# Kernel tuning notes

Hardware: AMD Instinct MI355X
Metric: run time of the kernel (lower is better)

## Reference

```python
import jax, jax.numpy as jnp
import numpy as np

N, T, D, H, W = 2, 1024, 1024, 16, 64  # batch, seq, embed, heads, temporal_window
DH = D // H                             # head_dim = 64
WIN = 2 * W + 1                         # 129


def setup_inputs() -> dict:
    key = jax.random.key(0)
    ks = jax.random.split(key, 10)
    s = 0.02
    inp = {"x": jax.random.normal(ks[0], (N, T, D), jnp.float32)}
    inp["w_q"] = jax.random.normal(ks[1], (D, D), jnp.float32) * s
    inp["b_q"] = jnp.zeros((D,), jnp.float32)
    inp["w_k"] = jax.random.normal(ks[2], (D, D), jnp.float32) * s
    inp["b_k"] = jnp.zeros((D,), jnp.float32)
    inp["w_v"] = jax.random.normal(ks[3], (D, D), jnp.float32) * s
    inp["b_v"] = jnp.zeros((D,), jnp.float32)
    inp["w_o"] = jax.random.normal(ks[4], (D, D), jnp.float32) * s
    inp["b_o"] = jnp.zeros((D,), jnp.float32)
    return inp


def reference(x, w_q, b_q, w_k, b_k, w_v, b_v, w_o, b_o):
    # x: (N, T, D). Windowed MHA: query t attends to positions [t-W, t+W].
    n, t_len, d = x.shape
    scale = 1.0 / jnp.sqrt(jnp.asarray(DH, x.dtype))

    q = (x @ w_q.T + b_q).reshape(n, t_len, H, DH)
    k = (x @ w_k.T + b_k).reshape(n, t_len, H, DH)
    v = (x @ w_v.T + b_v).reshape(n, t_len, H, DH)

    # window index map: pos[t, r] = t + r - W  (r in [0, 2W])
    t_idx = jnp.arange(t_len)[:, None]
    r_idx = jnp.arange(WIN)[None, :]
    pos = t_idx + r_idx - W
    valid = (pos >= 0) & (pos < t_len)
    idx = jnp.clip(pos, 0, t_len - 1)

    k_win = k[:, idx]
    v_win = v[:, idx]

    scores = jnp.einsum('nthd,ntwhd->nhtw', q, k_win) * scale
    scores = jnp.where(valid[None, None], scores, -jnp.inf)
    p = jax.nn.softmax(scores, axis=-1)

    out = jnp.einsum('nhtw,ntwhd->nthd', p, v_win).reshape(n, t_len, d)
    return out @ w_o.T + b_o
```

## Files before the change

### kernel.cpp

```cpp
#include <hip/hip_runtime.h>
#include <hip/hip_fp16.h>
#include <cstdint>
#include <cstddef>

using f16x8  = _Float16 __attribute__((ext_vector_type(8)));
using f16x4  = _Float16 __attribute__((ext_vector_type(4)));
using f32x4  = float __attribute__((ext_vector_type(4)));
using f32x16 = float __attribute__((ext_vector_type(16)));

#define GLDS16(g, l) __builtin_amdgcn_global_load_lds(                        \
    (const __attribute__((address_space(1))) void*)(g),                       \
    (__attribute__((address_space(3))) void*)(l), 16, 0, 0)

__device__ inline void cast4(const float* __restrict__ in,
                             _Float16* __restrict__ out, int i) {
  float4 v = reinterpret_cast<const float4*>(in)[i];
  f16x4 h;
  h[0] = (_Float16)v.x; h[1] = (_Float16)v.y;
  h[2] = (_Float16)v.z; h[3] = (_Float16)v.w;
  reinterpret_cast<f16x4*>(out)[i] = h;
}

__global__ void prep_kernel(const float* __restrict__ x,
                            const float* __restrict__ wq, const float* __restrict__ wk,
                            const float* __restrict__ wv, const float* __restrict__ wo,
                            const float* __restrict__ bq, const float* __restrict__ bk,
                            const float* __restrict__ bv,
                            _Float16* __restrict__ xh, _Float16* __restrict__ wcat,
                            _Float16* __restrict__ woh, float* __restrict__ bcat) {
  int i = blockIdx.x * blockDim.x + threadIdx.x;
  const int XU = 512 * 1024;
  const int WU = 256 * 1024;
  if (i < XU) { cast4(x, xh, i); return; }
  i -= XU;
  if (i < WU) { cast4(wq, wcat, i); return; }
  i -= WU;
  if (i < WU) { cast4(wk, wcat + 1024 * 1024, i); return; }
  i -= WU;
  if (i < WU) { cast4(wv, wcat + 2 * 1024 * 1024, i); return; }
  i -= WU;
  if (i < WU) { cast4(wo, woh, i); return; }
  i -= WU;
  if (i < 256) { reinterpret_cast<float4*>(bcat)[i] = reinterpret_cast<const float4*>(bq)[i]; return; }
  i -= 256;
  if (i < 256) { reinterpret_cast<float4*>(bcat + 1024)[i] = reinterpret_cast<const float4*>(bk)[i]; return; }
  i -= 256;
  if (i < 256) { reinterpret_cast<float4*>(bcat + 2048)[i] = reinterpret_cast<const float4*>(bv)[i]; return; }
}

template <int BM, int BN, typename TOUT>
__global__ __launch_bounds__(256, 4) void gemm_bt(
    const _Float16* __restrict__ A, const _Float16* __restrict__ B,
    const float* __restrict__ bias, TOUT* __restrict__ C,
    int M, int N, int K) {
  constexpr int AR = BM / 32;
  constexpr int BR = BN / 32;
  constexpr int MI = BM / 64;
  constexpr int NI = BN / 64;
  __shared__ _Float16 As[BM * 64];
  __shared__ _Float16 Bs[BN * 64];

  const int tid  = threadIdx.x;
  const int lane = tid & 63;
  const int wave = tid >> 6;
  const int l31  = lane & 31;
  const int half = lane >> 5;
  const int lsw  = l31 & 7;

  const int nlin = blockIdx.y * gridDim.x + blockIdx.x;
  const int xcd  = nlin & 7;
  const int slot = nlin >> 3;
  const int cpx  = gridDim.x >> 3;
  const int bx   = xcd * cpx + (slot % cpx);
  const int by   = slot / cpx;

  const int m0 = by * BM;
  const int n0 = bx * BN;
  const int wr = (wave >> 1) * (BM / 2);
  const int wc = (wave & 1) * (BN / 2);

  const int srow = tid >> 3;
  const int skun = (tid & 7) ^ (srow & 7);
  const _Float16* Ag[AR];
  const _Float16* Bg[BR];
#pragma unroll
  for (int r = 0; r < AR; r++) Ag[r] = A + (size_t)(m0 + 32 * r + srow) * K + skun * 8;
#pragma unroll
  for (int r = 0; r < BR; r++) Bg[r] = B + (size_t)(n0 + 32 * r + srow) * K + skun * 8;

  f32x16 acc[MI][NI];
#pragma unroll
  for (int i = 0; i < MI; i++)
#pragma unroll
    for (int j = 0; j < NI; j++) acc[i][j] = (f32x16)0.0f;

  for (int kt = 0; kt < K; kt += 64) {
    __syncthreads();
#pragma unroll
    for (int r = 0; r < AR; r++) GLDS16(Ag[r] + kt, &As[(256 * r + tid) * 8]);
#pragma unroll
    for (int r = 0; r < BR; r++) GLDS16(Bg[r] + kt, &Bs[(256 * r + tid) * 8]);
    __syncthreads();

#pragma unroll
    for (int ks = 0; ks < 4; ks++) {
      const int ku = ks * 2 + half;
      f16x8 af[MI], bf[NI];
#pragma unroll
      for (int mi = 0; mi < MI; mi++) {
        const int row = wr + mi * 32 + l31;
        af[mi] = *reinterpret_cast<const f16x8*>(&As[(row * 8 + (ku ^ lsw)) * 8]);
      }
#pragma unroll
      for (int ni = 0; ni < NI; ni++) {
        const int col = wc + ni * 32 + l31;
        bf[ni] = *reinterpret_cast<const f16x8*>(&Bs[(col * 8 + (ku ^ lsw)) * 8]);
      }
#pragma unroll
      for (int mi = 0; mi < MI; mi++)
#pragma unroll
        for (int ni = 0; ni < NI; ni++)
          acc[mi][ni] = __builtin_amdgcn_mfma_f32_32x32x16_f16(af[mi], bf[ni], acc[mi][ni], 0, 0, 0);
    }
  }

#pragma unroll
  for (int mi = 0; mi < MI; mi++) {
    const int rbase = m0 + wr + mi * 32 + 4 * half;
#pragma unroll
    for (int ni = 0; ni < NI; ni++) {
      const int col = n0 + wc + ni * 32 + l31;
      const float bv = bias ? bias[col] : 0.f;
#pragma unroll
      for (int r = 0; r < 16; r++) {
        const int row = rbase + (r & 3) + 8 * (r >> 2);
        C[(size_t)row * N + col] = (TOUT)(acc[mi][ni][r] + bv);
      }
    }
  }
}

#define T_LEN 1024
#define KSTR 72
#define VSTR 200

__global__ __launch_bounds__(256) void attn_win(
    const _Float16* __restrict__ qkv, _Float16* __restrict__ o) {
  __shared__ _Float16 KP[192 * KSTR];
  __shared__ _Float16 Vt[64 * VSTR];

  const int b  = blockIdx.x;
  const int qt = b & 15;
  const int h  = (b >> 4) & 15;
  const int n  = b >> 8;
  const int t0 = qt * 64;

  const int tid  = threadIdx.x;
  const int lane = tid & 63;
  const int wave = tid >> 6;
  const int l15  = lane & 15;
  const int quad = lane >> 4;
  const int jtb  = wave & 2;
  const int ksb  = wave >> 1;

  const size_t rowstr = 3072;
  const _Float16* qbase = qkv + (size_t)n * T_LEN * rowstr + h * 64;
  const _Float16* kbase = qbase + 1024;
  const _Float16* vbase = qbase + 2048;

  const _Float16* qrow = qbase + (size_t)(t0 + wave * 16 + l15) * rowstr;
  const f16x8 qf0 = *reinterpret_cast<const f16x8*>(qrow + quad * 8);
  const f16x8 qf1 = *reinterpret_cast<const f16x8*>(qrow + 32 + quad * 8);

  for (int idx = tid; idx < 192 * 8; idx += 256) {
    const int j  = idx >> 3;
    const int d8 = (idx & 7) * 8;
    const int t  = t0 - 64 + j;
    f16x8 kv;
    if (t >= 0 && t < T_LEN) {
      kv = *reinterpret_cast<const f16x8*>(kbase + (size_t)t * rowstr + d8);
    } else {
      for (int i = 0; i < 8; i++) kv[i] = (_Float16)0.f;
    }
    *reinterpret_cast<f16x8*>(&KP[j * KSTR + d8]) = kv;
  }
  for (int it = 0; it < 6; it++) {
    const int item = it * 256 + tid;
    const int j    = (item & 63) + ((item >> 9) << 6);
    const int dgrp = (item >> 6) & 7;
    const int t = t0 - 64 + j;
    f16x8 vv;
    if (t >= 0 && t < T_LEN) {
      vv = *reinterpret_cast<const f16x8*>(vbase + (size_t)t * rowstr + dgrp * 8);
    } else {
      for (int i = 0; i < 8; i++) vv[i] = (_Float16)0.f;
    }
#pragma unroll
    for (int i = 0; i < 8; i++) Vt[(dgrp * 8 + i) * VSTR + j] = vv[i];
  }
  __syncthreads();

  f32x4 accs[10];
#pragma unroll
  for (int t = 0; t < 10; t++) accs[t] = f32x4{0.f, 0.f, 0.f, 0.f};
#pragma unroll
  for (int t = 0; t < 10; t++) {
    const int jt = jtb + t;
    const f16x8 b0 = *reinterpret_cast<const f16x8*>(&KP[(jt * 16 + l15) * KSTR + quad * 8]);
    const f16x8 b1 = *reinterpret_cast<const f16x8*>(&KP[(jt * 16 + l15) * KSTR + 32 + quad * 8]);
    accs[t] = __builtin_amdgcn_mfma_f32_16x16x32_f16(qf0, b0, accs[t], 0, 0, 0);
    accs[t] = __builtin_amdgcn_mfma_f32_16x16x32_f16(qf1, b1, accs[t], 0, 0, 0);
  }
  __syncthreads();

  float rmax[4] = {-1e30f, -1e30f, -1e30f, -1e30f};
#pragma unroll
  for (int t = 0; t < 10; t++) {
    const int jcol = (jtb + t) * 16 + l15;
    const int tabs = t0 - 64 + jcol;
#pragma unroll
    for (int r = 0; r < 4; r++) {
      const int q = wave * 16 + quad * 4 + r;
      const bool valid = (jcol >= q) && (jcol <= q + 128) && (tabs >= 0) && (tabs < T_LEN);
      const float s = valid ? accs[t][r] * 0.125f : -1e30f;
      accs[t][r] = s;
      rmax[r] = fmaxf(rmax[r], s);
    }
  }
#pragma unroll
  for (int r = 0; r < 4; r++)
#pragma unroll
    for (int m = 1; m < 16; m <<= 1) rmax[r] = fmaxf(rmax[r], __shfl_xor(rmax[r], m));

  float rsum[4] = {0.f, 0.f, 0.f, 0.f};
#pragma unroll
  for (int t = 0; t < 10; t++)
#pragma unroll
    for (int r = 0; r < 4; r++) {
      const float p = __expf(accs[t][r] - rmax[r]);
      accs[t][r] = p;
      rsum[r] += p;
    }
#pragma unroll
  for (int r = 0; r < 4; r++)
#pragma unroll
    for (int m = 1; m < 16; m <<= 1) rsum[r] += __shfl_xor(rsum[r], m);

  _Float16* Pw = &KP[wave * 16 * VSTR];
#pragma unroll
  for (int t = 0; t < 10; t++)
#pragma unroll
    for (int r = 0; r < 4; r++)
      Pw[(quad * 4 + r) * VSTR + (jtb + t) * 16 + l15] = (_Float16)accs[t][r];
  __syncthreads();

  f32x4 acco[4];
#pragma unroll
  for (int ni = 0; ni < 4; ni++) acco[ni] = f32x4{0.f, 0.f, 0.f, 0.f};
#pragma unroll
  for (int ks2 = 0; ks2 < 5; ks2++) {
    const int ks = ksb + ks2;
    const f16x8 pa = *reinterpret_cast<const f16x8*>(&Pw[l15 * VSTR + ks * 32 + quad * 8]);
#pragma unroll
    for (int ni = 0; ni < 4; ni++) {
      const f16x8 vb = *reinterpret_cast<const f16x8*>(&Vt[(ni * 16 + l15) * VSTR + ks * 32 + quad * 8]);
      acco[ni] = __builtin_amdgcn_mfma_f32_16x16x32_f16(pa, vb, acco[ni], 0, 0, 0);
    }
  }

  float rinv[4];
#pragma unroll
  for (int r = 0; r < 4; r++) rinv[r] = 1.f / rsum[r];

  _Float16* obase = o + (size_t)(n * T_LEN + t0 + wave * 16) * 1024 + h * 64;
#pragma unroll
  for (int ni = 0; ni < 4; ni++)
#pragma unroll
    for (int r = 0; r < 4; r++)
      obase[(size_t)(quad * 4 + r) * 1024 + ni * 16 + l15] = (_Float16)(acco[ni][r] * rinv[r]);
}

extern "C" void kernel_launch(void* const* d_in, const int* in_sizes, int n_in,
                              void* d_out, int out_size, void* d_ws, size_t ws_size,
                              hipStream_t stream) {
  const float* x   = (const float*)d_in[0];
  const float* w_q = (const float*)d_in[1];
  const float* b_q = (const float*)d_in[2];
  const float* w_k = (const float*)d_in[3];
  const float* b_k = (const float*)d_in[4];
  const float* w_v = (const float*)d_in[5];
  const float* b_v = (const float*)d_in[6];
  const float* w_o = (const float*)d_in[7];
  const float* b_o = (const float*)d_in[8];
  float* out = (float*)d_out;

  char* ws = (char*)d_ws;
  _Float16* xh   = (_Float16*)(ws);
  _Float16* wcat = (_Float16*)(ws + (4ull << 20));
  _Float16* woh  = (_Float16*)(ws + (10ull << 20));
  _Float16* qkvh = (_Float16*)(ws + (12ull << 20));
  _Float16* oh   = xh;
  float*    bcat = (float*)(ws + (24ull << 20));

  const int PREP_UNITS = 512 * 1024 + 4 * 256 * 1024 + 3 * 256;
  prep_kernel<<<(PREP_UNITS + 255) / 256, 256, 0, stream>>>(
      x, w_q, w_k, w_v, w_o, b_q, b_k, b_v, xh, wcat, woh, bcat);

  gemm_bt<64, 128, _Float16><<<dim3(24, 32), 256, 0, stream>>>(
      xh, wcat, bcat, qkvh, 2048, 3072, 1024);

  attn_win<<<512, 256, 0, stream>>>(qkvh, oh);

  gemm_bt<64, 64, float><<<dim3(16, 32), 256, 0, stream>>>(
      oh, woh, b_o, out, 2048, 1024, 1024);
}
```

Before: 128.7 us.

## Use 2-wave GEMM blocks with wider per-wave tiles and paired V transpose stores

Reworks the GEMM kernel so each block runs 2 waves (128 threads). Each wave now covers the full BM rows and a WN-wide column slice, which gives more MFMA work per wave and more register reuse of fragments. Launch bounds change to match, and the global-to-LDS load loops are re-derived for the smaller thread count. Separately, the attention V transpose now loads two consecutive rows per thread and writes f16x2 pairs into the transposed LDS buffer, halving the number of LDS store instructions. The cost is fewer threads per block issuing loads and larger accumulator register use, which may hurt latency hiding.

```diff
diff --git a/kernel.cpp b/kernel.cpp
--- a/kernel.cpp
+++ b/kernel.cpp
@@ -5,6 +5,7 @@
 
 using f16x8  = _Float16 __attribute__((ext_vector_type(8)));
 using f16x4  = _Float16 __attribute__((ext_vector_type(4)));
+using f16x2  = _Float16 __attribute__((ext_vector_type(2)));
 using f32x4  = float __attribute__((ext_vector_type(4)));
 using f32x16 = float __attribute__((ext_vector_type(16)));
 
@@ -48,15 +49,18 @@
   if (i < 256) { reinterpret_cast<float4*>(bcat + 2048)[i] = reinterpret_cast<const float4*>(bv)[i]; return; }
 }
 
-template <int BM, int BN, typename TOUT>
-__global__ __launch_bounds__(256, 4) void gemm_bt(
+template <int BM, int BN, int WN, typename TOUT>
+__global__ __launch_bounds__((BN / WN) * 64, 2) void gemm_bt(
     const _Float16* __restrict__ A, const _Float16* __restrict__ B,
     const float* __restrict__ bias, TOUT* __restrict__ C,
     int M, int N, int K) {
-  constexpr int AR = BM / 32;
-  constexpr int BR = BN / 32;
-  constexpr int MI = BM / 64;
-  constexpr int NI = BN / 64;
+  constexpr int NW  = BN / WN;
+  constexpr int NT  = NW * 64;
+  constexpr int RPR = NT / 8;
+  constexpr int AR  = BM / RPR;
+  constexpr int BR  = BN / RPR;
+  constexpr int MI  = BM / 32;
+  constexpr int NI  = WN / 32;
   __shared__ _Float16 As[BM * 64];
   __shared__ _Float16 Bs[BN * 64];
 
@@ -76,17 +80,16 @@
 
   const int m0 = by * BM;
   const int n0 = bx * BN;
-  const int wr = (wave >> 1) * (BM / 2);
-  const int wc = (wave & 1) * (BN / 2);
+  const int wc = wave * WN;
 
   const int srow = tid >> 3;
   const int skun = (tid & 7) ^ (srow & 7);
   const _Float16* Ag[AR];
   const _Float16* Bg[BR];
 #pragma unroll
-  for (int r = 0; r < AR; r++) Ag[r] = A + (size_t)(m0 + 32 * r + srow) * K + skun * 8;
-#pragma unroll
-  for (int r = 0; r < BR; r++) Bg[r] = B + (size_t)(n0 + 32 * r + srow) * K + skun * 8;
+  for (int r = 0; r < AR; r++) Ag[r] = A + (size_t)(m0 + RPR * r + srow) * K + skun * 8;
+#pragma unroll
+  for (int r = 0; r < BR; r++) Bg[r] = B + (size_t)(n0 + RPR * r + srow) * K + skun * 8;
 
   f32x16 acc[MI][NI];
 #pragma unroll
@@ -97,9 +100,9 @@
   for (int kt = 0; kt < K; kt += 64) {
     __syncthreads();
 #pragma unroll
-    for (int r = 0; r < AR; r++) GLDS16(Ag[r] + kt, &As[(256 * r + tid) * 8]);
-#pragma unroll
-    for (int r = 0; r < BR; r++) GLDS16(Bg[r] + kt, &Bs[(256 * r + tid) * 8]);
+    for (int r = 0; r < AR; r++) GLDS16(Ag[r] + kt, &As[(NT * r + tid) * 8]);
+#pragma unroll
+    for (int r = 0; r < BR; r++) GLDS16(Bg[r] + kt, &Bs[(NT * r + tid) * 8]);
     __syncthreads();
 
 #pragma unroll
@@ -108,7 +111,7 @@
       f16x8 af[MI], bf[NI];
 #pragma unroll
       for (int mi = 0; mi < MI; mi++) {
-        const int row = wr + mi * 32 + l31;
+        const int row = mi * 32 + l31;
         af[mi] = *reinterpret_cast<const f16x8*>(&As[(row * 8 + (ku ^ lsw)) * 8]);
       }
 #pragma unroll
@@ -126,7 +129,7 @@
 
 #pragma unroll
   for (int mi = 0; mi < MI; mi++) {
-    const int rbase = m0 + wr + mi * 32 + 4 * half;
+    const int rbase = m0 + mi * 32 + 4 * half;
 #pragma unroll
     for (int ni = 0; ni < NI; ni++) {
       const int col = n0 + wc + ni * 32 + l31;
@@ -184,19 +187,28 @@
     }
     *reinterpret_cast<f16x8*>(&KP[j * KSTR + d8]) = kv;
   }
-  for (int it = 0; it < 6; it++) {
+  for (int it = 0; it < 3; it++) {
     const int item = it * 256 + tid;
-    const int j    = (item & 63) + ((item >> 9) << 6);
-    const int dgrp = (item >> 6) & 7;
-    const int t = t0 - 64 + j;
-    f16x8 vv;
-    if (t >= 0 && t < T_LEN) {
-      vv = *reinterpret_cast<const f16x8*>(vbase + (size_t)t * rowstr + dgrp * 8);
+    const int dg   = item / 96;
+    const int jp   = item - dg * 96;
+    const int j0   = 2 * jp;
+    const int ta   = t0 - 64 + j0;
+    f16x8 v0, v1;
+    if (ta >= 0 && ta < T_LEN) {
+      v0 = *reinterpret_cast<const f16x8*>(vbase + (size_t)ta * rowstr + dg * 8);
     } else {
-      for (int i = 0; i < 8; i++) vv[i] = (_Float16)0.f;
-    }
-#pragma unroll
-    for (int i = 0; i < 8; i++) Vt[(dgrp * 8 + i) * VSTR + j] = vv[i];
+      for (int i = 0; i < 8; i++) v0[i] = (_Float16)0.f;
+    }
+    if (ta + 1 >= 0 && ta + 1 < T_LEN) {
+      v1 = *reinterpret_cast<const f16x8*>(vbase + (size_t)(ta + 1) * rowstr + dg * 8);
+    } else {
+      for (int i = 0; i < 8; i++) v1[i] = (_Float16)0.f;
+    }
+#pragma unroll
+    for (int i = 0; i < 8; i++) {
+      f16x2 pr; pr[0] = v0[i]; pr[1] = v1[i];
+      *reinterpret_cast<f16x2*>(&Vt[(dg * 8 + i) * VSTR + j0]) = pr;
+    }
   }
   __syncthreads();
 
@@ -306,11 +318,11 @@
   prep_kernel<<<(PREP_UNITS + 255) / 256, 256, 0, stream>>>(
       x, w_q, w_k, w_v, w_o, b_q, b_k, b_v, xh, wcat, woh, bcat);
 
-  gemm_bt<64, 128, _Float16><<<dim3(24, 32), 256, 0, stream>>>(
+  gemm_bt<64, 128, 64, _Float16><<<dim3(24, 32), 128, 0, stream>>>(
       xh, wcat, bcat, qkvh, 2048, 3072, 1024);
 
   attn_win<<<512, 256, 0, stream>>>(qkvh, oh);
 
-  gemm_bt<64, 64, float><<<dim3(16, 32), 256, 0, stream>>>(
+  gemm_bt<64, 64, 32, float><<<dim3(16, 32), 128, 0, stream>>>(
       oh, woh, b_o, out, 2048, 1024, 1024);
 }
```

Result: slower. 134.1 us (+4.2%).
